# Kernel tuning notes

Hardware: AMD Instinct MI355X
Metric: run time of the kernel (lower is better)

Reference implementation:

```python
import jax, jax.numpy as jnp
import numpy as np

N = 100000   # nodes
E = 1600000  # edges (avg degree 16)
D = 128      # input channels
H = 128      # hidden channels
BN_EPS = 1e-5

def setup_inputs() -> dict:
    key = jax.random.key(0)
    ks = jax.random.split(key, 8)
    x = jax.random.normal(ks[0], (N, D), dtype=jnp.float32)
    edge_index = jax.random.randint(ks[1], (2, E), 0, N, dtype=jnp.int32)
    s = 0.02
    W1 = jax.random.normal(ks[2], (D, H), dtype=jnp.float32) * s
    b1 = jnp.zeros((H,), jnp.float32)
    g1 = jnp.ones((H,), jnp.float32)   # BN gamma
    be1 = jnp.zeros((H,), jnp.float32) # BN beta
    W2 = jax.random.normal(ks[3], (H, H), dtype=jnp.float32) * s
    b2 = jnp.zeros((H,), jnp.float32)
    g2 = jnp.ones((H,), jnp.float32)
    be2 = jnp.zeros((H,), jnp.float32)
    eps = jnp.zeros((), jnp.float32)   # trainable GIN eps, init 0
    return {"x": x, "edge_index": edge_index, "W1": W1, "b1": b1, "g1": g1,
            "be1": be1, "W2": W2, "b2": b2, "g2": g2, "be2": be2, "eps": eps}

def _bn_relu(h, gamma, beta):
    # BatchNorm1d in training mode: biased batch statistics over the node dim
    mu = jnp.mean(h, axis=0)
    var = jnp.mean(jnp.square(h - mu), axis=0)
    return jax.nn.relu((h - mu) * jax.lax.rsqrt(var + BN_EPS) * gamma + beta)

def reference(x, edge_index, W1, b1, g1, be1, W2, b2, g2, be2, eps):
    src, dst = edge_index[0], edge_index[1]
    # GIN neighbor aggregation: scatter-add of source features onto destinations
    agg = jax.ops.segment_sum(x[src], dst, num_segments=x.shape[0])  # [N, D]
    h = (1.0 + eps) * x + agg
    # 2-layer MLP: Linear -> BN -> ReLU, twice
    h = _bn_relu(h @ W1 + b1, g1, be1)
    h = _bn_relu(h @ W2 + b2, g2, be2)
    return h
```

## Files before the change

kernel.cpp:

```cpp
#include <hip/hip_runtime.h>

#define DIM 128
#define BINSHIFT 7
#define BINSZ 128
#define BCAP 2560
#define EPB 8192
#define NSL 8
#define SC 16

typedef __attribute__((ext_vector_type(8))) short bf16x8;
typedef __attribute__((ext_vector_type(4))) float f32x4;

__device__ inline unsigned short f2b(float f) {
    unsigned u = __builtin_bit_cast(unsigned, f);
    unsigned r = (u + 0x7FFFu + ((u >> 16) & 1u)) >> 16;
    return (unsigned short)r;
}
__device__ inline float b2f(unsigned short h) {
    unsigned u = ((unsigned)h) << 16;
    return __builtin_bit_cast(float, u);
}

__global__ __launch_bounds__(256)
void x_to_slices(const float* __restrict__ x, unsigned short* __restrict__ xbs, int N)
{
    int t = blockIdx.x * 256 + threadIdx.x;
    if (t >= N * NSL) return;
    int node = t >> 3, s = t & 7;
    const float* xp = x + (size_t)node * DIM + s * SC;
    float4 a = *(const float4*)(xp + 0);
    float4 b = *(const float4*)(xp + 4);
    float4 c = *(const float4*)(xp + 8);
    float4 d = *(const float4*)(xp + 12);
    unsigned short* o = xbs + ((size_t)s * N + node) * SC;
    bf16x8 o0, o1;
    o0[0]=(short)f2b(a.x); o0[1]=(short)f2b(a.y); o0[2]=(short)f2b(a.z); o0[3]=(short)f2b(a.w);
    o0[4]=(short)f2b(b.x); o0[5]=(short)f2b(b.y); o0[6]=(short)f2b(b.z); o0[7]=(short)f2b(b.w);
    o1[0]=(short)f2b(c.x); o1[1]=(short)f2b(c.y); o1[2]=(short)f2b(c.z); o1[3]=(short)f2b(c.w);
    o1[4]=(short)f2b(d.x); o1[5]=(short)f2b(d.y); o1[6]=(short)f2b(d.z); o1[7]=(short)f2b(d.w);
    *(bf16x8*)(o + 0) = o0;
    *(bf16x8*)(o + 8) = o1;
}

__global__ __launch_bounds__(1024)
void bin_edges(const int* __restrict__ src, const int* __restrict__ dst,
               unsigned* __restrict__ gcur, unsigned* __restrict__ binned,
               int E, int nbins)
{
    __shared__ unsigned hist[1024];
    __shared__ unsigned base[1024];
    const int t = threadIdx.x;
    const long long bb = (long long)blockIdx.x * EPB;
    if (t < nbins) hist[t] = 0;
    __syncthreads();

    unsigned pk[8], pos[8];
    int bn[8];
    bool ok[8];
    #pragma unroll
    for (int i = 0; i < 8; ++i) {
        long long idx = bb + i * 1024 + t;
        ok[i] = idx < E;
        if (ok[i]) {
            int s = src[idx], d = dst[idx];
            pk[i] = ((unsigned)(d & (BINSZ - 1)) << 17) | (unsigned)s;
            bn[i] = d >> BINSHIFT;
            pos[i] = atomicAdd(&hist[bn[i]], 1u);
        }
    }
    __syncthreads();
    if (t < nbins) base[t] = (unsigned)t * BCAP + atomicAdd(&gcur[t], hist[t]);
    __syncthreads();
    #pragma unroll
    for (int i = 0; i < 8; ++i) {
        if (ok[i]) {
            unsigned off = base[bn[i]] + pos[i];
            if (off < (unsigned)(bn[i] + 1) * BCAP) binned[off] = pk[i];
        }
    }
}

__global__ __launch_bounds__(512)
void bin_sort(const unsigned* __restrict__ gcur, const unsigned* __restrict__ binned,
              unsigned* __restrict__ srt, unsigned* __restrict__ gbase,
              unsigned* __restrict__ ghist)
{
    __shared__ unsigned hist[BINSZ];
    __shared__ unsigned base[BINSZ];
    __shared__ unsigned cur[BINSZ];
    const int t = threadIdx.x;
    const int bin = blockIdx.x;

    if (t < BINSZ) hist[t] = 0;
    __syncthreads();

    int cnt = (int)gcur[bin];
    if (cnt > BCAP) cnt = BCAP;
    const unsigned* __restrict__ bp = binned + (size_t)bin * BCAP;

    for (int i = t; i < cnt; i += 512)
        atomicAdd(&hist[(bp[i] >> 17) & (BINSZ - 1)], 1u);
    __syncthreads();
    if (t == 0) {
        unsigned run = 0;
        for (int i = 0; i < BINSZ; ++i) { base[i] = run; run += hist[i]; }
    }
    __syncthreads();
    if (t < BINSZ) cur[t] = base[t];
    __syncthreads();
    unsigned* __restrict__ sp = srt + (size_t)bin * BCAP;
    for (int i = t; i < cnt; i += 512) {
        unsigned p = bp[i];
        unsigned pos = atomicAdd(&cur[(p >> 17) & (BINSZ - 1)], 1u);
        sp[pos] = p & 0x1FFFFu;
    }
    if (t < BINSZ) {
        gbase[bin * BINSZ + t] = base[t];
        ghist[bin * BINSZ + t] = hist[t];
    }
}

__global__ __launch_bounds__(256)
void gather_slice(const unsigned short* __restrict__ xbs, const float* __restrict__ epsp,
                  const unsigned* __restrict__ gcur, const unsigned* __restrict__ srt,
                  const unsigned* __restrict__ gbase, const unsigned* __restrict__ ghist,
                  unsigned short* __restrict__ h0b, int N)
{
    __shared__ unsigned ssrt[BCAP];
    __shared__ unsigned sbase[BINSZ];
    __shared__ unsigned shist[BINSZ];
    const int t = threadIdx.x;
    const int bin = blockIdx.x >> 3;
    const int slice = blockIdx.x & 7;
    const int node0 = bin << BINSHIFT;

    int cnt = (int)gcur[bin];
    if (cnt > BCAP) cnt = BCAP;
    const unsigned* __restrict__ sp = srt + (size_t)bin * BCAP;
    for (int i = t; i < cnt; i += 256) ssrt[i] = sp[i];
    if (t < BINSZ) {
        sbase[t] = gbase[bin * BINSZ + t];
        shist[t] = ghist[bin * BINSZ + t];
    }
    __syncthreads();

    const float e = 1.0f + epsp[0];
    const int dn = t >> 1;
    const int c8 = (t & 1) * 8;
    const int node = node0 + dn;
    if (node >= N) return;

    const unsigned short* __restrict__ xs = xbs + (size_t)slice * N * SC + c8;
    bf16x8 v0 = *(const bf16x8*)(xs + (size_t)node * SC);
    float acc[8];
    #pragma unroll
    for (int q = 0; q < 8; ++q) acc[q] = e * b2f((unsigned short)v0[q]);

    const int b0 = (int)sbase[dn], hn = (int)shist[dn];
    int j = 0;
    for (; j + 4 <= hn; j += 4) {
        unsigned s0 = ssrt[b0 + j + 0];
        unsigned s1 = ssrt[b0 + j + 1];
        unsigned s2 = ssrt[b0 + j + 2];
        unsigned s3 = ssrt[b0 + j + 3];
        bf16x8 r0 = *(const bf16x8*)(xs + (size_t)s0 * SC);
        bf16x8 r1 = *(const bf16x8*)(xs + (size_t)s1 * SC);
        bf16x8 r2 = *(const bf16x8*)(xs + (size_t)s2 * SC);
        bf16x8 r3 = *(const bf16x8*)(xs + (size_t)s3 * SC);
        #pragma unroll
        for (int q = 0; q < 8; ++q)
            acc[q] += b2f((unsigned short)r0[q]) + b2f((unsigned short)r1[q])
                    + b2f((unsigned short)r2[q]) + b2f((unsigned short)r3[q]);
    }
    for (; j < hn; ++j) {
        unsigned s0 = ssrt[b0 + j];
        bf16x8 r0 = *(const bf16x8*)(xs + (size_t)s0 * SC);
        #pragma unroll
        for (int q = 0; q < 8; ++q) acc[q] += b2f((unsigned short)r0[q]);
    }
    bf16x8 o;
    #pragma unroll
    for (int q = 0; q < 8; ++q) o[q] = (short)f2b(acc[q]);
    *(bf16x8*)(h0b + (size_t)node * DIM + slice * SC + c8) = o;
}

template<bool APPLY_BN, bool OUT_BF16>
__global__ __launch_bounds__(1024)
void gemm_mfma(const unsigned short* __restrict__ A, const float* __restrict__ Wf,
               const float* __restrict__ bias, const float* __restrict__ ss,
               void* __restrict__ outp, float* __restrict__ stats, int N)
{
    __shared__ unsigned short sWT[128 * 128];
    __shared__ float red[256];
    const int tid = threadIdx.x;

    #pragma unroll
    for (int i = 0; i < 4; ++i) {
        int idx = (i * 1024 + tid) * 4;
        float4 w = *(const float4*)&Wf[idx];
        int k = idx >> 7, n0 = idx & 127;
        sWT[(n0 + 0) * 128 + (k ^ (((n0 + 0) & 7) << 3))] = f2b(w.x);
        sWT[(n0 + 1) * 128 + (k ^ (((n0 + 1) & 7) << 3))] = f2b(w.y);
        sWT[(n0 + 2) * 128 + (k ^ (((n0 + 2) & 7) << 3))] = f2b(w.z);
        sWT[(n0 + 3) * 128 + (k ^ (((n0 + 3) & 7) << 3))] = f2b(w.w);
    }
    if (tid < 256) red[tid] = 0.f;
    __syncthreads();

    const int lane = tid & 63;
    const int wave = tid >> 6;
    const int r0   = blockIdx.x * 256 + wave * 16;
    const int rl   = lane & 15;
    const int kg   = lane >> 4;
    int rr = r0 + rl;
    int rclamp = rr < N ? rr : N - 1;
    const unsigned short* arow = A + (size_t)rclamp * DIM + kg * 8;

    f32x4 acc[8];
    #pragma unroll
    for (int nt = 0; nt < 8; ++nt) acc[nt] = (f32x4)(0.f);

    #pragma unroll
    for (int kk = 0; kk < 128; kk += 32) {
        bf16x8 a8 = *(const bf16x8*)(arow + kk);
        if (APPLY_BN) {
            const float* sc = ss + kk + kg * 8;
            const float* sh = sc + DIM;
            bf16x8 tt;
            #pragma unroll
            for (int j = 0; j < 8; ++j) {
                float f = b2f((unsigned short)a8[j]) * sc[j] + sh[j];
                tt[j] = (short)f2b(fmaxf(f, 0.f));
            }
            a8 = tt;
        }
        const int ks = kk + kg * 8;
        #pragma unroll
        for (int nt = 0; nt < 8; ++nt) {
            int n = nt * 16 + rl;
            bf16x8 b8 = *(const bf16x8*)&sWT[n * 128 + (ks ^ ((n & 7) << 3))];
            acc[nt] = __builtin_amdgcn_mfma_f32_16x16x32_bf16(a8, b8, acc[nt], 0, 0, 0);
        }
    }

    const int orow0 = r0 + kg * 4;
    #pragma unroll
    for (int nt = 0; nt < 8; ++nt) {
        int n = nt * 16 + rl;
        float bb = bias[n];
        float ls = 0.f, ls2 = 0.f;
        #pragma unroll
        for (int j = 0; j < 4; ++j) {
            int r = orow0 + j;
            if (r < N) {
                float v = acc[nt][j] + bb;
                if (OUT_BF16) ((unsigned short*)outp)[(size_t)r * DIM + n] = f2b(v);
                else          ((float*)outp)[(size_t)r * DIM + n] = v;
                ls += v; ls2 += v * v;
            }
        }
        ls  += __shfl_xor(ls, 16);  ls  += __shfl_xor(ls, 32);
        ls2 += __shfl_xor(ls2, 16); ls2 += __shfl_xor(ls2, 32);
        if (kg == 0) { atomicAdd(&red[n], ls); atomicAdd(&red[128 + n], ls2); }
    }
    __syncthreads();
    if (tid < 256) atomicAdd(&stats[tid], red[tid]);
}

__global__ void bn_finalize(const float* __restrict__ stats, const float* __restrict__ gamma,
                            const float* __restrict__ beta, float* __restrict__ ss, float invN)
{
    int c = threadIdx.x;
    float mu  = stats[c] * invN;
    float var = stats[DIM + c] * invN - mu * mu;
    var = fmaxf(var, 0.f);
    float sc = gamma[c] * rsqrtf(var + 1e-5f);
    ss[c]       = sc;
    ss[DIM + c] = beta[c] - mu * sc;
}

__global__ __launch_bounds__(256)
void bn_relu_out_b(const unsigned short* __restrict__ h2b, const float* __restrict__ ss,
                   float* __restrict__ out, int n8)
{
    int i = blockIdx.x * 256 + threadIdx.x;
    if (i >= n8) return;
    int c = (i * 8) & 127;
    bf16x8 v = *(const bf16x8*)(h2b + (size_t)i * 8);
    float4 o0, o1;
    o0.x = fmaxf(b2f((unsigned short)v[0]) * ss[c+0] + ss[DIM+c+0], 0.f);
    o0.y = fmaxf(b2f((unsigned short)v[1]) * ss[c+1] + ss[DIM+c+1], 0.f);
    o0.z = fmaxf(b2f((unsigned short)v[2]) * ss[c+2] + ss[DIM+c+2], 0.f);
    o0.w = fmaxf(b2f((unsigned short)v[3]) * ss[c+3] + ss[DIM+c+3], 0.f);
    o1.x = fmaxf(b2f((unsigned short)v[4]) * ss[c+4] + ss[DIM+c+4], 0.f);
    o1.y = fmaxf(b2f((unsigned short)v[5]) * ss[c+5] + ss[DIM+c+5], 0.f);
    o1.z = fmaxf(b2f((unsigned short)v[6]) * ss[c+6] + ss[DIM+c+6], 0.f);
    o1.w = fmaxf(b2f((unsigned short)v[7]) * ss[c+7] + ss[DIM+c+7], 0.f);
    ((float4*)out)[i * 2 + 0] = o0;
    ((float4*)out)[i * 2 + 1] = o1;
}

extern "C" void kernel_launch(void* const* d_in, const int* in_sizes, int n_in,
                              void* d_out, int out_size, void* d_ws, size_t ws_size,
                              hipStream_t stream) {
    const float* x    = (const float*)d_in[0];
    const int*   ei   = (const int*)  d_in[1];
    const float* W1   = (const float*)d_in[2];
    const float* b1   = (const float*)d_in[3];
    const float* g1   = (const float*)d_in[4];
    const float* be1  = (const float*)d_in[5];
    const float* W2   = (const float*)d_in[6];
    const float* b2   = (const float*)d_in[7];
    const float* g2   = (const float*)d_in[8];
    const float* be2  = (const float*)d_in[9];
    const float* epsp = (const float*)d_in[10];
    float* out = (float*)d_out;

    const int N = in_sizes[0] / DIM;
    const int E = in_sizes[1] / 2;
    const int* src = ei;
    const int* dst = ei + E;
    const int nbins = (N + BINSZ - 1) >> BINSHIFT;

    const size_t SZ = (size_t)N * DIM * sizeof(unsigned short);
    char* w = (char*)d_ws;
    unsigned short* xbs = (unsigned short*)w;
    unsigned short* h1b = xbs;
    unsigned short* h0b = (unsigned short*)(w + SZ);
    unsigned short* h2b = h0b;
    unsigned* binned = (unsigned*)(w + 2 * SZ);
    unsigned* srt    = binned + (size_t)nbins * BCAP;
    unsigned* gbase  = srt + (size_t)nbins * BCAP;
    unsigned* ghist  = gbase + (size_t)nbins * BINSZ;
    unsigned* gcur   = ghist + (size_t)nbins * BINSZ;
    float* stats1 = (float*)(gcur + 1024);
    float* stats2 = stats1 + 256;
    float* ss1    = stats2 + 256;
    float* ss2    = ss1 + 256;

    hipMemsetAsync(gcur, 0, (1024 + 512) * sizeof(unsigned), stream);

    x_to_slices<<<(N * NSL + 255) / 256, 256, 0, stream>>>(x, xbs, N);
    bin_edges<<<(E + EPB - 1) / EPB, 1024, 0, stream>>>(src, dst, gcur, binned, E, nbins);
    bin_sort<<<nbins, 512, 0, stream>>>(gcur, binned, srt, gbase, ghist);
    gather_slice<<<nbins * NSL, 256, 0, stream>>>(xbs, epsp, gcur, srt, gbase, ghist, h0b, N);

    const int gblocks = (N + 255) / 256;
    gemm_mfma<false, true><<<gblocks, 1024, 0, stream>>>(h0b, W1, b1, nullptr, h1b, stats1, N);
    bn_finalize<<<1, DIM, 0, stream>>>(stats1, g1, be1, ss1, 1.0f / (float)N);
    gemm_mfma<true, true><<<gblocks, 1024, 0, stream>>>(h1b, W2, b2, ss1, h2b, stats2, N);
    bn_finalize<<<1, DIM, 0, stream>>>(stats2, g2, be2, ss2, 1.0f / (float)N);
    const int n8 = N * DIM / 8;
    bn_relu_out_b<<<(n8 + 255) / 256, 256, 0, stream>>>(h2b, ss2, out, n8);
}
```

Baseline: 203.3 us.

## Replace sliced bf16 layout and per-slice gather with row-major CSR gather

```diff
diff --git a/kernel.cpp b/kernel.cpp
--- a/kernel.cpp
+++ b/kernel.cpp
@@ -5,8 +5,6 @@
 #define BINSZ 128
 #define BCAP 2560
 #define EPB 8192
-#define NSL 8
-#define SC 16
 
 typedef __attribute__((ext_vector_type(8))) short bf16x8;
 typedef __attribute__((ext_vector_type(4))) float f32x4;
@@ -22,24 +20,16 @@
 }
 
 __global__ __launch_bounds__(256)
-void x_to_slices(const float* __restrict__ x, unsigned short* __restrict__ xbs, int N)
-{
-    int t = blockIdx.x * 256 + threadIdx.x;
-    if (t >= N * NSL) return;
-    int node = t >> 3, s = t & 7;
-    const float* xp = x + (size_t)node * DIM + s * SC;
-    float4 a = *(const float4*)(xp + 0);
-    float4 b = *(const float4*)(xp + 4);
-    float4 c = *(const float4*)(xp + 8);
-    float4 d = *(const float4*)(xp + 12);
-    unsigned short* o = xbs + ((size_t)s * N + node) * SC;
-    bf16x8 o0, o1;
-    o0[0]=(short)f2b(a.x); o0[1]=(short)f2b(a.y); o0[2]=(short)f2b(a.z); o0[3]=(short)f2b(a.w);
-    o0[4]=(short)f2b(b.x); o0[5]=(short)f2b(b.y); o0[6]=(short)f2b(b.z); o0[7]=(short)f2b(b.w);
-    o1[0]=(short)f2b(c.x); o1[1]=(short)f2b(c.y); o1[2]=(short)f2b(c.z); o1[3]=(short)f2b(c.w);
-    o1[4]=(short)f2b(d.x); o1[5]=(short)f2b(d.y); o1[6]=(short)f2b(d.z); o1[7]=(short)f2b(d.w);
-    *(bf16x8*)(o + 0) = o0;
-    *(bf16x8*)(o + 8) = o1;
+void x_to_bf16(const float* __restrict__ x, unsigned short* __restrict__ xb, int n8)
+{
+    int i = blockIdx.x * 256 + threadIdx.x;
+    if (i >= n8) return;
+    float4 a = ((const float4*)x)[i * 2];
+    float4 b = ((const float4*)x)[i * 2 + 1];
+    bf16x8 o;
+    o[0] = (short)f2b(a.x); o[1] = (short)f2b(a.y); o[2] = (short)f2b(a.z); o[3] = (short)f2b(a.w);
+    o[4] = (short)f2b(b.x); o[5] = (short)f2b(b.y); o[6] = (short)f2b(b.z); o[7] = (short)f2b(b.w);
+    ((bf16x8*)xb)[i] = o;
 }
 
 __global__ __launch_bounds__(1024)
@@ -120,68 +110,52 @@
     }
 }
 
-__global__ __launch_bounds__(256)
-void gather_slice(const unsigned short* __restrict__ xbs, const float* __restrict__ epsp,
-                  const unsigned* __restrict__ gcur, const unsigned* __restrict__ srt,
-                  const unsigned* __restrict__ gbase, const unsigned* __restrict__ ghist,
-                  unsigned short* __restrict__ h0b, int N)
-{
-    __shared__ unsigned ssrt[BCAP];
-    __shared__ unsigned sbase[BINSZ];
-    __shared__ unsigned shist[BINSZ];
+__global__ __launch_bounds__(512)
+void gather_csr(const unsigned short* __restrict__ xb, const float* __restrict__ epsp,
+                const unsigned* __restrict__ srt, const unsigned* __restrict__ gbase,
+                const unsigned* __restrict__ ghist,
+                unsigned short* __restrict__ h0b, int N)
+{
     const int t = threadIdx.x;
-    const int bin = blockIdx.x >> 3;
-    const int slice = blockIdx.x & 7;
-    const int node0 = bin << BINSHIFT;
-
-    int cnt = (int)gcur[bin];
-    if (cnt > BCAP) cnt = BCAP;
-    const unsigned* __restrict__ sp = srt + (size_t)bin * BCAP;
-    for (int i = t; i < cnt; i += 256) ssrt[i] = sp[i];
-    if (t < BINSZ) {
-        sbase[t] = gbase[bin * BINSZ + t];
-        shist[t] = ghist[bin * BINSZ + t];
-    }
-    __syncthreads();
-
+    const int node = blockIdx.x * 32 + (t >> 4);
+    if (node >= N) return;
+    const int g = (t & 15) * 8;
     const float e = 1.0f + epsp[0];
-    const int dn = t >> 1;
-    const int c8 = (t & 1) * 8;
-    const int node = node0 + dn;
-    if (node >= N) return;
-
-    const unsigned short* __restrict__ xs = xbs + (size_t)slice * N * SC + c8;
-    bf16x8 v0 = *(const bf16x8*)(xs + (size_t)node * SC);
+
+    bf16x8 v0 = *(const bf16x8*)(xb + (size_t)node * DIM + g);
     float acc[8];
     #pragma unroll
     for (int q = 0; q < 8; ++q) acc[q] = e * b2f((unsigned short)v0[q]);
 
-    const int b0 = (int)sbase[dn], hn = (int)shist[dn];
+    const int b0 = (int)gbase[node];
+    const int hn = (int)ghist[node];
+    const unsigned* __restrict__ sp = srt + (size_t)(node >> BINSHIFT) * BCAP + b0;
+
     int j = 0;
     for (; j + 4 <= hn; j += 4) {
-        unsigned s0 = ssrt[b0 + j + 0];
-        unsigned s1 = ssrt[b0 + j + 1];
-        unsigned s2 = ssrt[b0 + j + 2];
-        unsigned s3 = ssrt[b0 + j + 3];
-        bf16x8 r0 = *(const bf16x8*)(xs + (size_t)s0 * SC);
-        bf16x8 r1 = *(const bf16x8*)(xs + (size_t)s1 * SC);
-        bf16x8 r2 = *(const bf16x8*)(xs + (size_t)s2 * SC);
-        bf16x8 r3 = *(const bf16x8*)(xs + (size_t)s3 * SC);
+        unsigned s0 = sp[j + 0];
+        unsigned s1 = sp[j + 1];
+        unsigned s2 = sp[j + 2];
+        unsigned s3 = sp[j + 3];
+        bf16x8 r0 = *(const bf16x8*)(xb + (size_t)s0 * DIM + g);
+        bf16x8 r1 = *(const bf16x8*)(xb + (size_t)s1 * DIM + g);
+        bf16x8 r2 = *(const bf16x8*)(xb + (size_t)s2 * DIM + g);
+        bf16x8 r3 = *(const bf16x8*)(xb + (size_t)s3 * DIM + g);
         #pragma unroll
         for (int q = 0; q < 8; ++q)
             acc[q] += b2f((unsigned short)r0[q]) + b2f((unsigned short)r1[q])
                     + b2f((unsigned short)r2[q]) + b2f((unsigned short)r3[q]);
     }
     for (; j < hn; ++j) {
-        unsigned s0 = ssrt[b0 + j];
-        bf16x8 r0 = *(const bf16x8*)(xs + (size_t)s0 * SC);
+        unsigned s0 = sp[j];
+        bf16x8 r0 = *(const bf16x8*)(xb + (size_t)s0 * DIM + g);
         #pragma unroll
         for (int q = 0; q < 8; ++q) acc[q] += b2f((unsigned short)r0[q]);
     }
     bf16x8 o;
     #pragma unroll
     for (int q = 0; q < 8; ++q) o[q] = (short)f2b(acc[q]);
-    *(bf16x8*)(h0b + (size_t)node * DIM + slice * SC + c8) = o;
+    *(bf16x8*)(h0b + (size_t)node * DIM + g) = o;
 }
 
 template<bool APPLY_BN, bool OUT_BF16>
@@ -324,15 +298,15 @@
 
     const size_t SZ = (size_t)N * DIM * sizeof(unsigned short);
     char* w = (char*)d_ws;
-    unsigned short* xbs = (unsigned short*)w;
-    unsigned short* h1b = xbs;
+    unsigned short* xb  = (unsigned short*)w;
     unsigned short* h0b = (unsigned short*)(w + SZ);
     unsigned short* h2b = h0b;
+    unsigned short* h1b = (unsigned short*)(w + 2 * SZ);
     unsigned* binned = (unsigned*)(w + 2 * SZ);
     unsigned* srt    = binned + (size_t)nbins * BCAP;
     unsigned* gbase  = srt + (size_t)nbins * BCAP;
     unsigned* ghist  = gbase + (size_t)nbins * BINSZ;
-    unsigned* gcur   = ghist + (size_t)nbins * BINSZ;
+    unsigned* gcur   = (unsigned*)(w + 3 * SZ);
     float* stats1 = (float*)(gcur + 1024);
     float* stats2 = stats1 + 256;
     float* ss1    = stats2 + 256;
@@ -340,16 +314,16 @@
 
     hipMemsetAsync(gcur, 0, (1024 + 512) * sizeof(unsigned), stream);
 
-    x_to_slices<<<(N * NSL + 255) / 256, 256, 0, stream>>>(x, xbs, N);
+    const int n8 = N * DIM / 8;
+    x_to_bf16<<<(n8 + 255) / 256, 256, 0, stream>>>(x, xb, n8);
     bin_edges<<<(E + EPB - 1) / EPB, 1024, 0, stream>>>(src, dst, gcur, binned, E, nbins);
     bin_sort<<<nbins, 512, 0, stream>>>(gcur, binned, srt, gbase, ghist);
-    gather_slice<<<nbins * NSL, 256, 0, stream>>>(xbs, epsp, gcur, srt, gbase, ghist, h0b, N);
+    gather_csr<<<(N + 31) / 32, 512, 0, stream>>>(xb, epsp, srt, gbase, ghist, h0b, N);
 
     const int gblocks = (N + 255) / 256;
     gemm_mfma<false, true><<<gblocks, 1024, 0, stream>>>(h0b, W1, b1, nullptr, h1b, stats1, N);
     bn_finalize<<<1, DIM, 0, stream>>>(stats1, g1, be1, ss1, 1.0f / (float)N);
     gemm_mfma<true, true><<<gblocks, 1024, 0, stream>>>(h1b, W2, b2, ss1, h2b, stats2, N);
     bn_finalize<<<1, DIM, 0, stream>>>(stats2, g2, be2, ss2, 1.0f / (float)N);
-    const int n8 = N * DIM / 8;
     bn_relu_out_b<<<(n8 + 255) / 256, 256, 0, stream>>>(h2b, ss2, out, n8);
 }
```

Measured after the change: 187.6 us. 7.7% less time.
